# Performance work log

Measured on AMD Instinct MI355X. Metric: run time of the kernel, lower is better.

The kernel has to match this reference:

```python
import jax, jax.numpy as jnp
import numpy as np

B, N, C = 4, 2048, 768
H = 12
HD = C // H
SCALE = HD ** -0.5


def setup_inputs() -> dict:
    key = jax.random.key(0)
    k1, k2, k3 = jax.random.split(key, 3)
    x = jax.random.normal(k1, (B, N, C), dtype=jnp.float32)
    w_qkv = jax.random.normal(k2, (3 * C, C), dtype=jnp.float32) * (C ** -0.5)
    w_proj = jax.random.normal(k3, (C, C), dtype=jnp.float32) * (C ** -0.5)
    b_proj = jnp.zeros((C,), dtype=jnp.float32)
    return {"x": x, "w_qkv": w_qkv, "w_proj": w_proj, "b_proj": b_proj}


def reference(x, w_qkv, w_proj, b_proj):
    Bx, Nx, Cx = x.shape
    # qkv linear: x @ W^T -> [B, N, 3C], then split into heads
    qkv = jnp.einsum('bnc,dc->bnd', x, w_qkv)
    qkv = qkv.reshape(Bx, Nx, 3, H, HD).transpose(2, 0, 3, 1, 4)  # [3, B, H, N, HD]
    q, k, v = qkv[0], qkv[1], qkv[2]
    attn = jnp.einsum('bhqd,bhkd->bhqk', q, k) * SCALE  # [B, H, N, N]
    attn = jax.nn.softmax(attn, axis=-1)
    out = jnp.einsum('bhqk,bhkd->bhqd', attn, v)  # [B, H, N, HD]
    out = out.transpose(0, 2, 1, 3).reshape(Bx, Nx, Cx)
    out = jnp.einsum('bnc,dc->bnd', out, w_proj) + b_proj
    return out
```

## Files before the change

### kernel.cpp

```cpp
#include <hip/hip_runtime.h>
#include <hip/hip_bf16.h>
#include <stdint.h>

#define DI __device__ __forceinline__

typedef __bf16 bf16x8 __attribute__((ext_vector_type(8)));
typedef float f32x4 __attribute__((ext_vector_type(4)));
typedef unsigned short u16;

DI u16 f2bf(float f) {
  union { float f; uint32_t u; } x; x.f = f;
  uint32_t r = (x.u + 0x7FFFu + ((x.u >> 16) & 1u)) >> 16;
  return (u16)r;
}
DI bf16x8 load16(const u16* p) { return *(const bf16x8*)p; }

DI void async_copy16(void* lds, const void* g) {
  __builtin_amdgcn_global_load_lds(
      (const __attribute__((address_space(1))) uint32_t*)g,
      (__attribute__((address_space(3))) uint32_t*)lds, 16, 0, 0);
}

DI f32x4 mfma16(bf16x8 a, bf16x8 b, f32x4 c) {
  return __builtin_amdgcn_mfma_f32_16x16x32_bf16(a, b, c, 0, 0, 0);
}

DI float redsum16(float v) {
  v += __shfl_xor(v, 1);
  v += __shfl_xor(v, 2);
  v += __shfl_xor(v, 4);
  v += __shfl_xor(v, 8);
  return v;
}

#define QSCALE (0.125f * 1.44269504088896340736f)

__global__ __launch_bounds__(256)
void cvt_f32_bf16(const float* __restrict__ src, u16* __restrict__ dst, int n) {
  int i = (blockIdx.x * 256 + threadIdx.x) * 4;
  if (i < n) {
    float4 v = *(const float4*)(src + i);
    ushort4 o;
    o.x = f2bf(v.x); o.y = f2bf(v.y); o.z = f2bf(v.z); o.w = f2bf(v.w);
    *(ushort4*)(dst + i) = o;
  }
}

__global__ __launch_bounds__(256)
void gemm_qkv(const u16* __restrict__ A, const u16* __restrict__ Bm,
              u16* __restrict__ Qb, u16* __restrict__ Kb, u16* __restrict__ Vt,
              int M, int N, int K) {
  __shared__ u16 As[128 * 32];
  __shared__ u16 Bs[128 * 32];

  const int tid  = threadIdx.x;
  const int lane = tid & 63;
  const int wave = tid >> 6;
  const int m0 = blockIdx.y * 128;
  const int n0 = blockIdx.x * 128;
  const int wm = (wave & 1) * 64;
  const int wn = (wave >> 1) * 64;
  const int c = lane & 15;
  const int g = lane >> 4;

  f32x4 acc[4][4] = {};

  for (int k0 = 0; k0 < K; k0 += 32) {
#pragma unroll
    for (int i = 0; i < 2; ++i) {
      int j = i * 256 + tid;
      int row = j >> 2;
      int col = (j & 3) * 8;
      async_copy16(&As[j * 8], &A[(size_t)(m0 + row) * K + k0 + col]);
      async_copy16(&Bs[j * 8], &Bm[(size_t)(n0 + row) * K + k0 + col]);
    }
    __syncthreads();

    bf16x8 af[4], bfr[4];
#pragma unroll
    for (int t = 0; t < 4; ++t) {
      af[t]  = *(const bf16x8*)&As[(wm + t * 16 + c) * 32 + g * 8];
      bfr[t] = *(const bf16x8*)&Bs[(wn + t * 16 + c) * 32 + g * 8];
    }
#pragma unroll
    for (int mt = 0; mt < 4; ++mt)
#pragma unroll
      for (int nt = 0; nt < 4; ++nt)
        acc[mt][nt] = mfma16(af[mt], bfr[nt], acc[mt][nt]);
    __syncthreads();
  }

  if (n0 < 768) {
#pragma unroll
    for (int nt = 0; nt < 4; ++nt) {
      int col = n0 + wn + nt * 16 + c;
#pragma unroll
      for (int mt = 0; mt < 4; ++mt)
#pragma unroll
        for (int r = 0; r < 4; ++r) {
          int row = m0 + wm + mt * 16 + g * 4 + r;
          Qb[(size_t)row * 768 + col] = f2bf(acc[mt][nt][r] * QSCALE);
        }
    }
  } else if (n0 < 1536) {
#pragma unroll
    for (int nt = 0; nt < 4; ++nt) {
      int col = n0 - 768 + wn + nt * 16 + c;
#pragma unroll
      for (int mt = 0; mt < 4; ++mt)
#pragma unroll
        for (int r = 0; r < 4; ++r) {
          int row = m0 + wm + mt * 16 + g * 4 + r;
          Kb[(size_t)row * 768 + col] = f2bf(acc[mt][nt][r]);
        }
    }
  } else {
#pragma unroll
    for (int nt = 0; nt < 4; ++nt) {
      int cv = n0 - 1536 + wn + nt * 16 + c;
      int hv = cv >> 6, d = cv & 63;
#pragma unroll
      for (int mt = 0; mt < 4; ++mt) {
        int row = m0 + wm + mt * 16 + g * 4;
        int b = row >> 11, nn = row & 2047;
        ushort4 o;
        o.x = f2bf(acc[mt][nt][0]); o.y = f2bf(acc[mt][nt][1]);
        o.z = f2bf(acc[mt][nt][2]); o.w = f2bf(acc[mt][nt][3]);
        *(ushort4*)&Vt[(((size_t)b * 12 + hv) * 64 + d) * 2048 + nn] = o;
      }
    }
  }
}

__global__ __launch_bounds__(256)
void gemm_proj(const u16* __restrict__ A, const u16* __restrict__ Bm,
               const float* __restrict__ bias, float* __restrict__ Co,
               int M, int N, int K) {
  __shared__ u16 As[128 * 32];
  __shared__ u16 Bs[128 * 32];

  const int tid  = threadIdx.x;
  const int lane = tid & 63;
  const int wave = tid >> 6;
  const int m0 = blockIdx.y * 128;
  const int n0 = blockIdx.x * 128;
  const int wm = (wave & 1) * 64;
  const int wn = (wave >> 1) * 64;
  const int c = lane & 15;
  const int g = lane >> 4;

  f32x4 acc[4][4] = {};

  for (int k0 = 0; k0 < K; k0 += 32) {
#pragma unroll
    for (int i = 0; i < 2; ++i) {
      int j = i * 256 + tid;
      int row = j >> 2;
      int col = (j & 3) * 8;
      async_copy16(&As[j * 8], &A[(size_t)(m0 + row) * K + k0 + col]);
      async_copy16(&Bs[j * 8], &Bm[(size_t)(n0 + row) * K + k0 + col]);
    }
    __syncthreads();

    bf16x8 af[4], bfr[4];
#pragma unroll
    for (int t = 0; t < 4; ++t) {
      af[t]  = *(const bf16x8*)&As[(wm + t * 16 + c) * 32 + g * 8];
      bfr[t] = *(const bf16x8*)&Bs[(wn + t * 16 + c) * 32 + g * 8];
    }
#pragma unroll
    for (int mt = 0; mt < 4; ++mt)
#pragma unroll
      for (int nt = 0; nt < 4; ++nt)
        acc[mt][nt] = mfma16(af[mt], bfr[nt], acc[mt][nt]);
    __syncthreads();
  }

#pragma unroll
  for (int nt = 0; nt < 4; ++nt) {
    int col = n0 + wn + nt * 16 + c;
    float bv = bias[col];
#pragma unroll
    for (int mt = 0; mt < 4; ++mt)
#pragma unroll
      for (int r = 0; r < 4; ++r) {
        int row = m0 + wm + mt * 16 + g * 4 + r;
        Co[(size_t)row * N + col] = acc[mt][nt][r] + bv;
      }
  }
}

__global__ __launch_bounds__(256)
void attn_flash(const u16* __restrict__ Qb, const u16* __restrict__ Kb,
                const u16* __restrict__ Vt, u16* __restrict__ out) {
  __shared__ u16 Ks[2 * 64 * 32];
  __shared__ u16 Vs[2 * 64 * 32];
  __shared__ __align__(16) u16 Plds[4][16 * 72];

  const int tid  = threadIdx.x;
  const int lane = tid & 63;
  const int wave = tid >> 6;
  const int idx = blockIdx.x;
  const int qchunk = idx & 31;
  const int h = (idx >> 5) % 12;
  const int b = idx / (32 * 12);
  const int q0 = qchunk * 64 + wave * 16;
  const int c = lane & 15;
  const int g = lane >> 4;

  const u16* Qp = Qb + (size_t)b * 2048 * 768 + h * 64;
  const u16* Kp = Kb + (size_t)b * 2048 * 768 + h * 64;
  const u16* Vp = Vt + ((size_t)b * 12 + h) * 64 * 2048;

  u16* pw = &Plds[wave][0];

  const bf16x8 qf0 = load16(&Qp[(size_t)(q0 + c) * 768 + g * 8]);
  const bf16x8 qf1 = load16(&Qp[(size_t)(q0 + c) * 768 + 32 + g * 8]);

  const int j0 = tid, j1 = tid + 256;

  float lsum[4] = {0.f, 0.f, 0.f, 0.f};
  f32x4 o[4] = {};

  for (int k0 = 0; k0 < 2048; k0 += 64) {
    {
      int half0 = j0 >> 8, kk0 = (j0 >> 2) & 63, ch0 = j0 & 3;
      int half1 = j1 >> 8, kk1 = (j1 >> 2) & 63, ch1 = j1 & 3;
      async_copy16(&Ks[j0 * 8], &Kp[(size_t)(k0 + kk0) * 768 + half0 * 32 + ch0 * 8]);
      async_copy16(&Ks[j1 * 8], &Kp[(size_t)(k0 + kk1) * 768 + half1 * 32 + ch1 * 8]);
      async_copy16(&Vs[j0 * 8], &Vp[(size_t)((j0 >> 2) & 63) * 2048 + k0 + half0 * 32 + ch0 * 8]);
      async_copy16(&Vs[j1 * 8], &Vp[(size_t)((j1 >> 2) & 63) * 2048 + k0 + half1 * 32 + ch1 * 8]);
    }
    __syncthreads();

    f32x4 s[4] = {};
#pragma unroll
    for (int kt = 0; kt < 4; ++kt) {
      bf16x8 kf0 = *(const bf16x8*)&Ks[(kt * 16 + c) * 32 + g * 8];
      bf16x8 kf1 = *(const bf16x8*)&Ks[64 * 32 + (kt * 16 + c) * 32 + g * 8];
      s[kt] = mfma16(qf0, kf0, s[kt]);
      s[kt] = mfma16(qf1, kf1, s[kt]);
    }

#pragma unroll
    for (int kt = 0; kt < 4; ++kt)
#pragma unroll
      for (int r = 0; r < 4; ++r) {
        float p = __builtin_amdgcn_exp2f(s[kt][r]);
        lsum[r] += p;
        pw[(g * 4 + r) * 72 + kt * 16 + c] = f2bf(p);
      }
    __asm__ volatile("s_waitcnt lgkmcnt(0)" ::: "memory");

#pragma unroll
    for (int kt2 = 0; kt2 < 2; ++kt2) {
      const bf16x8 pf = *(const bf16x8*)&pw[c * 72 + kt2 * 32 + g * 8];
#pragma unroll
      for (int dt = 0; dt < 4; ++dt) {
        bf16x8 vf = *(const bf16x8*)&Vs[kt2 * 64 * 32 + (dt * 16 + c) * 32 + g * 8];
        o[dt] = mfma16(pf, vf, o[dt]);
      }
    }
    __syncthreads();
  }

  float inv[4];
#pragma unroll
  for (int r = 0; r < 4; ++r) inv[r] = 1.f / redsum16(lsum[r]);
#pragma unroll
  for (int dt = 0; dt < 4; ++dt)
#pragma unroll
    for (int r = 0; r < 4; ++r) {
      int n = q0 + g * 4 + r;
      out[(size_t)(b * 2048 + n) * 768 + h * 64 + dt * 16 + c] =
          f2bf(o[dt][r] * inv[r]);
    }
}

extern "C" void kernel_launch(void* const* d_in, const int* in_sizes, int n_in,
                              void* d_out, int out_size, void* d_ws, size_t ws_size,
                              hipStream_t stream) {
  const float* x      = (const float*)d_in[0];
  const float* w_qkv  = (const float*)d_in[1];
  const float* w_proj = (const float*)d_in[2];
  const float* b_proj = (const float*)d_in[3];
  float* out = (float*)d_out;

  const int M = 8192;
  const int C = 768;
  const int NQKV = 2304;

  u16* xb     = (u16*)d_ws;
  u16* wqkvb  = xb + (size_t)M * C;
  u16* wprojb = wqkvb + (size_t)NQKV * C;
  u16* Qb     = wprojb + (size_t)C * C;
  u16* Kb     = Qb + (size_t)M * C;
  u16* Vt     = Kb + (size_t)M * C;
  u16* attn   = Vt + (size_t)M * C;

  dim3 blk(256);
  cvt_f32_bf16<<<dim3(M * C / 1024), blk, 0, stream>>>(x, xb, M * C);
  cvt_f32_bf16<<<dim3(NQKV * C / 1024), blk, 0, stream>>>(w_qkv, wqkvb, NQKV * C);
  cvt_f32_bf16<<<dim3(C * C / 1024), blk, 0, stream>>>(w_proj, wprojb, C * C);

  gemm_qkv<<<dim3(NQKV / 128, M / 128), blk, 0, stream>>>(
      xb, wqkvb, Qb, Kb, Vt, M, NQKV, C);
  attn_flash<<<dim3(4 * 12 * 32), blk, 0, stream>>>(Qb, Kb, Vt, attn);
  gemm_proj<<<dim3(C / 128, M / 128), blk, 0, stream>>>(
      attn, wprojb, b_proj, out, M, C, C);
}
```

Measured before the change: 258.7 us.

## Process 32 query rows per wave in attention and merge conversion kernels

Each attention wave now handles two 16-row query tiles that share each K/V tile loaded to LDS, so a workgroup covers 128 queries. This halves the grid and the K/V global traffic per query. The three fp32-to-bf16 conversion launches are merged into one kernel, and exp results are packed with a paired bf16 conversion. The cost is more registers per wave and fewer workgroups, 768 instead of 1536, which may lower occupancy.

New measurement: 234.8 us. 9.3% less time.

```diff
diff --git a/kernel.cpp b/kernel.cpp
--- a/kernel.cpp
+++ b/kernel.cpp
@@ -33,17 +33,28 @@
   return v;
 }
 
+DI uint32_t pk_bf16(float a, float b) {
+  union { __hip_bfloat162 v; uint32_t u; } r;
+  r.v = __float22bfloat162_rn(make_float2(a, b));
+  return r.u;
+}
+
 #define QSCALE (0.125f * 1.44269504088896340736f)
 
 __global__ __launch_bounds__(256)
-void cvt_f32_bf16(const float* __restrict__ src, u16* __restrict__ dst, int n) {
+void cvt_all(const float* __restrict__ s0, u16* __restrict__ d0, int n0,
+             const float* __restrict__ s1, u16* __restrict__ d1, int n1,
+             const float* __restrict__ s2, u16* __restrict__ d2, int n2) {
   int i = (blockIdx.x * 256 + threadIdx.x) * 4;
-  if (i < n) {
-    float4 v = *(const float4*)(src + i);
-    ushort4 o;
-    o.x = f2bf(v.x); o.y = f2bf(v.y); o.z = f2bf(v.z); o.w = f2bf(v.w);
-    *(ushort4*)(dst + i) = o;
-  }
+  const float* s; u16* d;
+  if (i < n0) { s = s0 + i; d = d0 + i; }
+  else if (i < n0 + n1) { s = s1 + (i - n0); d = d1 + (i - n0); }
+  else if (i < n0 + n1 + n2) { s = s2 + (i - n0 - n1); d = d2 + (i - n0 - n1); }
+  else return;
+  float4 v = *(const float4*)s;
+  ushort4 o;
+  o.x = f2bf(v.x); o.y = f2bf(v.y); o.z = f2bf(v.z); o.w = f2bf(v.w);
+  *(ushort4*)d = o;
 }
 
 __global__ __launch_bounds__(256)
@@ -195,16 +206,16 @@
                 const u16* __restrict__ Vt, u16* __restrict__ out) {
   __shared__ u16 Ks[2 * 64 * 32];
   __shared__ u16 Vs[2 * 64 * 32];
-  __shared__ __align__(16) u16 Plds[4][16 * 72];
+  __shared__ __align__(16) u16 Plds[4][32 * 72];
 
   const int tid  = threadIdx.x;
   const int lane = tid & 63;
   const int wave = tid >> 6;
   const int idx = blockIdx.x;
-  const int qchunk = idx & 31;
-  const int h = (idx >> 5) % 12;
-  const int b = idx / (32 * 12);
-  const int q0 = qchunk * 64 + wave * 16;
+  const int qchunk = idx & 15;
+  const int h = (idx >> 4) % 12;
+  const int b = idx / (16 * 12);
+  const int q0 = qchunk * 128 + wave * 32;
   const int c = lane & 15;
   const int g = lane >> 4;
 
@@ -216,64 +227,86 @@
 
   const bf16x8 qf0 = load16(&Qp[(size_t)(q0 + c) * 768 + g * 8]);
   const bf16x8 qf1 = load16(&Qp[(size_t)(q0 + c) * 768 + 32 + g * 8]);
+  const bf16x8 qg0 = load16(&Qp[(size_t)(q0 + 16 + c) * 768 + g * 8]);
+  const bf16x8 qg1 = load16(&Qp[(size_t)(q0 + 16 + c) * 768 + 32 + g * 8]);
 
   const int j0 = tid, j1 = tid + 256;
 
-  float lsum[4] = {0.f, 0.f, 0.f, 0.f};
-  f32x4 o[4] = {};
+  float lsum0[4] = {0.f, 0.f, 0.f, 0.f};
+  float lsum1[4] = {0.f, 0.f, 0.f, 0.f};
+  f32x4 o0[4] = {}, o1[4] = {};
 
   for (int k0 = 0; k0 < 2048; k0 += 64) {
     {
-      int half0 = j0 >> 8, kk0 = (j0 >> 2) & 63, ch0 = j0 & 3;
-      int half1 = j1 >> 8, kk1 = (j1 >> 2) & 63, ch1 = j1 & 3;
-      async_copy16(&Ks[j0 * 8], &Kp[(size_t)(k0 + kk0) * 768 + half0 * 32 + ch0 * 8]);
-      async_copy16(&Ks[j1 * 8], &Kp[(size_t)(k0 + kk1) * 768 + half1 * 32 + ch1 * 8]);
-      async_copy16(&Vs[j0 * 8], &Vp[(size_t)((j0 >> 2) & 63) * 2048 + k0 + half0 * 32 + ch0 * 8]);
-      async_copy16(&Vs[j1 * 8], &Vp[(size_t)((j1 >> 2) & 63) * 2048 + k0 + half1 * 32 + ch1 * 8]);
-    }
-    __syncthreads();
-
-    f32x4 s[4] = {};
+      int kk0 = (j0 >> 2) & 63, ch0 = j0 & 3;
+      int kk1 = (j1 >> 2) & 63, ch1 = j1 & 3;
+      async_copy16(&Ks[j0 * 8], &Kp[(size_t)(k0 + kk0) * 768 + ch0 * 8]);
+      async_copy16(&Ks[j1 * 8], &Kp[(size_t)(k0 + kk1) * 768 + 32 + ch1 * 8]);
+      async_copy16(&Vs[j0 * 8], &Vp[(size_t)kk0 * 2048 + k0 + ch0 * 8]);
+      async_copy16(&Vs[j1 * 8], &Vp[(size_t)kk1 * 2048 + k0 + 32 + ch1 * 8]);
+    }
+    __syncthreads();
+
+    f32x4 s0[4] = {}, s1[4] = {};
 #pragma unroll
     for (int kt = 0; kt < 4; ++kt) {
       bf16x8 kf0 = *(const bf16x8*)&Ks[(kt * 16 + c) * 32 + g * 8];
       bf16x8 kf1 = *(const bf16x8*)&Ks[64 * 32 + (kt * 16 + c) * 32 + g * 8];
-      s[kt] = mfma16(qf0, kf0, s[kt]);
-      s[kt] = mfma16(qf1, kf1, s[kt]);
-    }
-
-#pragma unroll
-    for (int kt = 0; kt < 4; ++kt)
-#pragma unroll
-      for (int r = 0; r < 4; ++r) {
-        float p = __builtin_amdgcn_exp2f(s[kt][r]);
-        lsum[r] += p;
-        pw[(g * 4 + r) * 72 + kt * 16 + c] = f2bf(p);
+      s0[kt] = mfma16(qf0, kf0, s0[kt]);
+      s0[kt] = mfma16(qf1, kf1, s0[kt]);
+      s1[kt] = mfma16(qg0, kf0, s1[kt]);
+      s1[kt] = mfma16(qg1, kf1, s1[kt]);
+    }
+
+#pragma unroll
+    for (int kt = 0; kt < 4; ++kt) {
+#pragma unroll
+      for (int r2 = 0; r2 < 2; ++r2) {
+        float pa = __builtin_amdgcn_exp2f(s0[kt][r2 * 2]);
+        float pb = __builtin_amdgcn_exp2f(s0[kt][r2 * 2 + 1]);
+        lsum0[r2 * 2] += pa; lsum0[r2 * 2 + 1] += pb;
+        union { uint32_t u; u16 h[2]; } pk; pk.u = pk_bf16(pa, pb);
+        pw[(g * 4 + r2 * 2) * 72 + kt * 16 + c]     = pk.h[0];
+        pw[(g * 4 + r2 * 2 + 1) * 72 + kt * 16 + c] = pk.h[1];
+        float qa = __builtin_amdgcn_exp2f(s1[kt][r2 * 2]);
+        float qb = __builtin_amdgcn_exp2f(s1[kt][r2 * 2 + 1]);
+        lsum1[r2 * 2] += qa; lsum1[r2 * 2 + 1] += qb;
+        union { uint32_t u; u16 h[2]; } qk; qk.u = pk_bf16(qa, qb);
+        pw[(16 + g * 4 + r2 * 2) * 72 + kt * 16 + c]     = qk.h[0];
+        pw[(16 + g * 4 + r2 * 2 + 1) * 72 + kt * 16 + c] = qk.h[1];
       }
+    }
     __asm__ volatile("s_waitcnt lgkmcnt(0)" ::: "memory");
 
 #pragma unroll
     for (int kt2 = 0; kt2 < 2; ++kt2) {
-      const bf16x8 pf = *(const bf16x8*)&pw[c * 72 + kt2 * 32 + g * 8];
+      const bf16x8 pf0 = *(const bf16x8*)&pw[c * 72 + kt2 * 32 + g * 8];
+      const bf16x8 pf1 = *(const bf16x8*)&pw[(16 + c) * 72 + kt2 * 32 + g * 8];
 #pragma unroll
       for (int dt = 0; dt < 4; ++dt) {
         bf16x8 vf = *(const bf16x8*)&Vs[kt2 * 64 * 32 + (dt * 16 + c) * 32 + g * 8];
-        o[dt] = mfma16(pf, vf, o[dt]);
+        o0[dt] = mfma16(pf0, vf, o0[dt]);
+        o1[dt] = mfma16(pf1, vf, o1[dt]);
       }
     }
     __syncthreads();
   }
 
-  float inv[4];
-#pragma unroll
-  for (int r = 0; r < 4; ++r) inv[r] = 1.f / redsum16(lsum[r]);
+  float inv0[4], inv1[4];
+#pragma unroll
+  for (int r = 0; r < 4; ++r) {
+    inv0[r] = 1.f / redsum16(lsum0[r]);
+    inv1[r] = 1.f / redsum16(lsum1[r]);
+  }
 #pragma unroll
   for (int dt = 0; dt < 4; ++dt)
 #pragma unroll
     for (int r = 0; r < 4; ++r) {
       int n = q0 + g * 4 + r;
       out[(size_t)(b * 2048 + n) * 768 + h * 64 + dt * 16 + c] =
-          f2bf(o[dt][r] * inv[r]);
+          f2bf(o0[dt][r] * inv0[r]);
+      out[(size_t)(b * 2048 + n + 16) * 768 + h * 64 + dt * 16 + c] =
+          f2bf(o1[dt][r] * inv1[r]);
     }
 }
 
@@ -299,13 +332,13 @@
   u16* attn   = Vt + (size_t)M * C;
 
   dim3 blk(256);
-  cvt_f32_bf16<<<dim3(M * C / 1024), blk, 0, stream>>>(x, xb, M * C);
-  cvt_f32_bf16<<<dim3(NQKV * C / 1024), blk, 0, stream>>>(w_qkv, wqkvb, NQKV * C);
-  cvt_f32_bf16<<<dim3(C * C / 1024), blk, 0, stream>>>(w_proj, wprojb, C * C);
+  const int n0 = M * C, n1 = NQKV * C, n2 = C * C;
+  cvt_all<<<dim3((n0 + n1 + n2) / 1024), blk, 0, stream>>>(
+      x, xb, n0, w_qkv, wqkvb, n1, w_proj, wprojb, n2);
 
   gemm_qkv<<<dim3(NQKV / 128, M / 128), blk, 0, stream>>>(
       xb, wqkvb, Qb, Kb, Vt, M, NQKV, C);
-  attn_flash<<<dim3(4 * 12 * 32), blk, 0, stream>>>(Qb, Kb, Vt, attn);
+  attn_flash<<<dim3(4 * 12 * 16), blk, 0, stream>>>(Qb, Kb, Vt, attn);
   gemm_proj<<<dim3(C / 128, M / 128), blk, 0, stream>>>(
       attn, wprojb, b_proj, out, M, C, C);
 }
```
